# Performance work log

Measured on AMD Instinct MI355X. Metric: run time of the kernel, lower is better.

The kernel has to match this reference:

```python
import jax, jax.numpy as jnp
import numpy as np

BLOCK = 128          # fp8 quantization block size (from linear_deepseek_v3)
FP8_MAX = 448.0      # max representable value of float8_e4m3fn
F8 = jnp.float8_e4m3fn
G, T, K, N = 8, 1024, 7168, 2048


def setup_inputs() -> dict:
    key = jax.random.key(0)
    kx, kw, kb = jax.random.split(key, 3)
    xs = jax.random.normal(kx, (G, T, K), jnp.float32)
    # Build an fp8 block-quantized weight + per-(128x128)-block fp32 scale,
    # matching the stored self.weight (fp8) and self.scale parameters.
    w_raw = jax.random.normal(kw, (G, N, K), jnp.float32)
    wb = w_raw.reshape(G, N // BLOCK, BLOCK, K // BLOCK, BLOCK)
    amax = jnp.max(jnp.abs(wb), axis=(2, 4))            # [G, NB, KB]
    scale = amax / FP8_MAX
    w_q = (wb / scale[:, :, None, :, None]).astype(F8).astype(jnp.float32)
    weight = w_q.reshape(G, N, K)                        # fp8 code values held in fp32
    bias = jax.random.normal(kb, (G, N), jnp.float32) * 0.02
    return {"xs": xs, "weight": weight, "scale": scale, "bias": bias}


def reference(xs, weight, scale, bias):
    """Grouped fp8 block-quantized GEMM with inline dequant.
    xs:     [G, T, K] fp32 activations (one slab per group)
    weight: [G, N, K] fp8-quantized weights (stored as fp32 code values)
    scale:  [G, N/128, K/128] fp32 per-block weight scales
    bias:   [G, N] fp32
    """
    g, t, k = xs.shape
    n = weight.shape[1]
    kb, nb = k // BLOCK, n // BLOCK
    # --- act_quant_deepseek_v3: per (token, 128-col block) absmax/448 scale ---
    xb = xs.reshape(g, t, kb, BLOCK)
    a_scale = jnp.max(jnp.abs(xb), axis=-1) / FP8_MAX        # [G, T, KB]
    x_q = (xb / a_scale[..., None]).astype(F8).astype(jnp.float32)
    x_deq = (x_q * a_scale[..., None]).reshape(g, t, k)      # fused dequant
    # --- weight dequant: broadcast per-(128x128)-block scale ---
    w_deq = (weight.reshape(g, nb, BLOCK, kb, BLOCK)
             * scale[:, :, None, :, None]).reshape(g, n, k)
    # --- grouped GEMM (y = x A^T) + bias, fp32 accumulation ---
    y = jnp.einsum('gtk,gnk->gtn', x_deq, w_deq) + bias[:, None, :]
    return y
```

## Files before the change

kernel.cpp:

```cpp
#include <hip/hip_runtime.h>
#include <hip/hip_bf16.h>
#include <stdint.h>

#define G_ 8
#define T_ 1024
#define K_ 7168
#define N_ 2048
#define KB_ 56
#define NB_ 16
#define NT8_ 56

#define ACT_WGS  57344
#define WREC_WGS 28672

typedef __attribute__((ext_vector_type(4))) float f32x4;
typedef __attribute__((ext_vector_type(8))) int   i32x8;

typedef __attribute__((address_space(3))) uint32_t lds_u32_t;
typedef const __attribute__((address_space(1))) uint32_t gbl_u32_t;

__device__ __forceinline__ void gload_lds16(const void* gsrc, const void* ldst)
{
    __builtin_amdgcn_global_load_lds(
        (gbl_u32_t*)(uintptr_t)gsrc,
        (lds_u32_t*)(uint32_t)(uintptr_t)ldst, 16, 0, 0);
}

__device__ __forceinline__ void blockbar()
{
    asm volatile("" ::: "memory");
    __builtin_amdgcn_s_barrier();
    asm volatile("" ::: "memory");
}

__global__ __launch_bounds__(256) void prep_kernel(
    const float* __restrict__ xs, uint8_t* __restrict__ xq8,
    float* __restrict__ ascale,
    const float* __restrict__ w, uint8_t* __restrict__ wq8)
{
    const int bid = blockIdx.x;
    const int tid = threadIdx.x;
    if (bid < ACT_WGS) {
        const int grp = (bid * 256 + tid) >> 5;
        const int l   = tid & 31;
        const size_t base = (size_t)grp * 128 + (size_t)l * 4;

        const float4 v = *(const float4*)(xs + base);
        float am = fmaxf(fmaxf(fabsf(v.x), fabsf(v.y)),
                         fmaxf(fabsf(v.z), fabsf(v.w)));
#pragma unroll
        for (int off = 1; off <= 16; off <<= 1)
            am = fmaxf(am, __shfl_xor(am, off, 64));

        const float rs = 448.0f / am;
        const float s  = am * (1.0f / 448.0f);

        int pk = __builtin_amdgcn_cvt_pk_fp8_f32(v.x * rs, v.y * rs, 0, false);
        pk     = __builtin_amdgcn_cvt_pk_fp8_f32(v.z * rs, v.w * rs, pk, true);
        *(uint32_t*)(xq8 + base) = (uint32_t)pk;

        if (l == 0) {
            const int kb = grp % KB_;
            const int t  = (grp / KB_) & (T_ - 1);
            const int g  = grp / (KB_ * T_);
            ascale[(((size_t)(g * 4 + (t >> 8))) * KB_ + kb) * 256 + (t & 255)] = s;
        }
    } else {
        const size_t i = ((size_t)(bid - ACT_WGS) * 256 + tid) * 16;
        uint32_t o[4];
#pragma unroll
        for (int q = 0; q < 4; ++q) {
            const float4 a = *(const float4*)(w + i + q * 4);
            int pk = __builtin_amdgcn_cvt_pk_fp8_f32(a.x, a.y, 0, false);
            pk     = __builtin_amdgcn_cvt_pk_fp8_f32(a.z, a.w, pk, true);
            o[q] = (uint32_t)pk;
        }
        *(uint4*)(wq8 + i) = make_uint4(o[0], o[1], o[2], o[3]);
    }
}

union Frag { i32x8 v; struct { int4 lo, hi; } p; };

#define RD_FRAG(dst, base, r)                                                 \
  { const int rx_ = ((r) & 7) << 4;                                           \
    const char* bp_ = smem + (base) + (r)*128;                                \
    dst.p.lo = *(const int4*)(bp_ + ((lhi*32) ^ rx_));                        \
    dst.p.hi = *(const int4*)(bp_ + ((lhi*32 + 16) ^ rx_)); }

#define STG_A(c, t, bb) gload_lds16(pA8[c] + (size_t)(t)*128,                 \
      smem + (bb)*16384 + (c)*4096 + tid*16)
#define STG_B(c, t, bb) gload_lds16(pB8[c] + (size_t)(t)*128,                 \
      smem + 32768 + (bb)*16384 + (c)*4096 + tid*16)
#define STG_S(c) gload_lds16(pS + (size_t)(c)*2048,                           \
      smem + 65536 + ((c)&1)*4096 + tid*16)

__global__ __launch_bounds__(256, 2) void gemm_fp8_kernel(
    const uint8_t* __restrict__ xq8, const uint8_t* __restrict__ wq8,
    const float* __restrict__ ascale, const float* __restrict__ wscale,
    const float* __restrict__ bias, float* __restrict__ y)
{
    __shared__ char smem[73952];

    const int bx0 = blockIdx.x;
    const int g     = bx0 & 7;
    const int inner = bx0 >> 3;
    const int tn    = inner & 15;
    const int tm    = inner >> 4;
    const int t0 = tm * 128, n0 = tn * 128;

    const int tid = threadIdx.x, lane = tid & 63, wid = tid >> 6;
    const int l15 = lane & 15, lhi = lane >> 4;
    const int wrow = (wid >> 1) * 64;
    const int wcol = (wid & 1) * 64;

    const uint8_t* Ag = xq8 + (size_t)g * T_ * K_;
    const uint8_t* Bg = wq8 + (size_t)g * N_ * K_;

    const int srow = tid >> 3;
    const int xoff = ((tid & 7) ^ (srow & 7)) * 16;
    const uint8_t* pA8[4];
    const uint8_t* pB8[4];
#pragma unroll
    for (int c = 0; c < 4; ++c) {
        pA8[c] = Ag + (size_t)(t0 + c * 32 + srow) * K_ + xoff;
        pB8[c] = Bg + (size_t)(n0 + c * 32 + srow) * K_ + xoff;
    }

    const float* pS = ascale + ((size_t)(g * 4 + (tm >> 1)) * KB_) * 256
                    + (tid >> 5) * 256 + (tm & 1) * 128 + (tid & 31) * 4;

    const f32x4 z4 = {0.f, 0.f, 0.f, 0.f};
    f32x4 acc[4][4] = {};
    Frag aF[4], bF[4];
    f32x4 asv[4];

    if (tid < KB_) {
        const float wv = wscale[((size_t)(g * NB_ + tn)) * KB_ + tid];
        *(float*)(smem + 73728 + tid * 4) = wv;
    }
    STG_S(0);
#pragma unroll
    for (int c = 0; c < 4; ++c) { STG_A(c, 0, 0); STG_B(c, 0, 0); }
    asm volatile("s_waitcnt vmcnt(0)" ::: "memory");
    asm volatile("s_waitcnt lgkmcnt(0)" ::: "memory");
    blockbar();

    for (int u = 0; u < NT8_; ++u) {
        const int cur = u & 1, nxt = cur ^ 1;
        const bool pf = (u + 1 < NT8_);
        const int sbuf = (u >> 3) & 1;

        if ((u & 7) == 0 && u + 8 < NT8_) STG_S((u >> 3) + 1);
        if (pf) {
#pragma unroll
            for (int c = 0; c < 4; ++c) { STG_A(c, u + 1, nxt); STG_B(c, u + 1, nxt); }
        }

        const float wsc = *(const float*)(smem + 73728 + u * 4);

#pragma unroll
        for (int n = 0; n < 4; ++n)
            RD_FRAG(bF[n], 32768 + cur * 16384, wcol + n * 16 + l15);
#pragma unroll
        for (int m = 0; m < 4; ++m)
            RD_FRAG(aF[m], cur * 16384, wrow + m * 16 + l15);
#pragma unroll
        for (int m = 0; m < 4; ++m) {
            const float4 sv = *(const float4*)(smem + 65536 + sbuf * 4096 +
                (u & 7) * 512 + (wrow + m * 16 + lhi * 4) * 4);
            asv[m][0] = sv.x * wsc; asv[m][1] = sv.y * wsc;
            asv[m][2] = sv.z * wsc; asv[m][3] = sv.w * wsc;
        }

        __builtin_amdgcn_s_setprio(1);
#pragma unroll
        for (int m = 0; m < 4; ++m) {
#pragma unroll
            for (int n = 0; n < 4; ++n) {
                f32x4 blk = __builtin_amdgcn_mfma_scale_f32_16x16x128_f8f6f4(
                    aF[m].v, bF[n].v, z4, 0, 0, 0, 0x7F7F7F7F, 0, 0x7F7F7F7F);
                acc[m][n] += blk * asv[m];
            }
        }
        __builtin_amdgcn_s_setprio(0);

        if (pf) {
            asm volatile("s_waitcnt vmcnt(0)" ::: "memory");
            blockbar();
        }
    }

    float* Yg = y + (size_t)g * T_ * N_;
#pragma unroll
    for (int n = 0; n < 4; ++n) {
        const int col = n0 + wcol + n * 16 + l15;
        const float bv = bias[g * N_ + col];
#pragma unroll
        for (int m = 0; m < 4; ++m) {
            const int r0 = t0 + wrow + m * 16 + lhi * 4;
#pragma unroll
            for (int j = 0; j < 4; ++j)
                Yg[(size_t)(r0 + j) * N_ + col] = acc[m][n][j] + bv;
        }
    }
}

extern "C" void kernel_launch(void* const* d_in, const int* in_sizes, int n_in,
                              void* d_out, int out_size, void* d_ws, size_t ws_size,
                              hipStream_t stream)
{
    const float* xs     = (const float*)d_in[0];
    const float* weight = (const float*)d_in[1];
    const float* scale  = (const float*)d_in[2];
    const float* bias   = (const float*)d_in[3];
    float* y = (float*)d_out;

    uint8_t* xq8  = (uint8_t*)d_ws;
    float*   ascl = (float*)((char*)d_ws + 58720256);
    uint8_t* wq8  = (uint8_t*)((char*)d_ws + 60555264);

    prep_kernel<<<ACT_WGS + WREC_WGS, 256, 0, stream>>>(
        xs, xq8, ascl, weight, wq8);

    gemm_fp8_kernel<<<G_ * (T_ / 128) * (N_ / 128), 256, 0, stream>>>(
        xq8, wq8, ascl, scale, bias, y);
}
```

Before: 349.2 us.

## Warp-specialize GEMM into producer/consumer waves with triple-buffered LDS

The GEMM block grows to 512 threads. Four producer waves issue the global-to-LDS loads and four consumer waves do the MFMA work, and the LDS ring goes from double to triple buffering with loads issued two steps ahead. The tile order also changes so adjacent blocks share N tiles. The aim is to hide global load latency behind compute. In exchange occupancy drops to one block per CU, LDS use grows, and half the waves never do MFMA work.

After: 326.3 us. -6.5%, faster.

```diff
diff --git a/kernel.cpp b/kernel.cpp
--- a/kernel.cpp
+++ b/kernel.cpp
@@ -88,27 +88,29 @@
     dst.p.hi = *(const int4*)(bp_ + ((lhi*32 + 16) ^ rx_)); }
 
 #define STG_A(c, t, bb) gload_lds16(pA8[c] + (size_t)(t)*128,                 \
-      smem + (bb)*16384 + (c)*4096 + tid*16)
+      smem + (bb)*16384 + (c)*4096 + ptid*16)
 #define STG_B(c, t, bb) gload_lds16(pB8[c] + (size_t)(t)*128,                 \
-      smem + 32768 + (bb)*16384 + (c)*4096 + tid*16)
+      smem + 49152 + (bb)*16384 + (c)*4096 + ptid*16)
 #define STG_S(c) gload_lds16(pS + (size_t)(c)*2048,                           \
-      smem + 65536 + ((c)&1)*4096 + tid*16)
-
-__global__ __launch_bounds__(256, 2) void gemm_fp8_kernel(
+      smem + 98304 + ((c)&1)*4096 + ptid*16)
+
+__global__ __launch_bounds__(512, 1) void gemm_fp8_kernel(
     const uint8_t* __restrict__ xq8, const uint8_t* __restrict__ wq8,
     const float* __restrict__ ascale, const float* __restrict__ wscale,
     const float* __restrict__ bias, float* __restrict__ y)
 {
-    __shared__ char smem[73952];
+    __shared__ char smem[106752];
 
     const int bx0 = blockIdx.x;
     const int g     = bx0 & 7;
     const int inner = bx0 >> 3;
-    const int tn    = inner & 15;
-    const int tm    = inner >> 4;
+    const int tm    = inner & 7;
+    const int tn    = inner >> 3;
     const int t0 = tm * 128, n0 = tn * 128;
 
-    const int tid = threadIdx.x, lane = tid & 63, wid = tid >> 6;
+    const int tid  = threadIdx.x, lane = tid & 63, wid = tid >> 6;
+    const bool producer = (wid >= 4);
+    const int ptid = tid & 255;
     const int l15 = lane & 15, lhi = lane >> 4;
     const int wrow = (wid >> 1) * 64;
     const int wcol = (wid & 1) * 64;
@@ -116,8 +118,8 @@
     const uint8_t* Ag = xq8 + (size_t)g * T_ * K_;
     const uint8_t* Bg = wq8 + (size_t)g * N_ * K_;
 
-    const int srow = tid >> 3;
-    const int xoff = ((tid & 7) ^ (srow & 7)) * 16;
+    const int srow = ptid >> 3;
+    const int xoff = ((ptid & 7) ^ (srow & 7)) * 16;
     const uint8_t* pA8[4];
     const uint8_t* pB8[4];
 #pragma unroll
@@ -125,82 +127,90 @@
         pA8[c] = Ag + (size_t)(t0 + c * 32 + srow) * K_ + xoff;
         pB8[c] = Bg + (size_t)(n0 + c * 32 + srow) * K_ + xoff;
     }
-
     const float* pS = ascale + ((size_t)(g * 4 + (tm >> 1)) * KB_) * 256
-                    + (tid >> 5) * 256 + (tm & 1) * 128 + (tid & 31) * 4;
+                    + (ptid >> 5) * 256 + (tm & 1) * 128 + (ptid & 31) * 4;
 
     const f32x4 z4 = {0.f, 0.f, 0.f, 0.f};
     f32x4 acc[4][4] = {};
-    Frag aF[4], bF[4];
+    Frag bF[4];
     f32x4 asv[4];
 
-    if (tid < KB_) {
-        const float wv = wscale[((size_t)(g * NB_ + tn)) * KB_ + tid];
-        *(float*)(smem + 73728 + tid * 4) = wv;
-    }
-    STG_S(0);
-#pragma unroll
-    for (int c = 0; c < 4; ++c) { STG_A(c, 0, 0); STG_B(c, 0, 0); }
-    asm volatile("s_waitcnt vmcnt(0)" ::: "memory");
-    asm volatile("s_waitcnt lgkmcnt(0)" ::: "memory");
+    if (producer) {
+        if (ptid < KB_) {
+            const float wv = wscale[((size_t)(g * NB_ + tn)) * KB_ + ptid];
+            *(float*)(smem + 106496 + ptid * 4) = wv;
+        }
+        STG_S(0);
+#pragma unroll
+        for (int c = 0; c < 4; ++c) { STG_A(c, 0, 0); STG_B(c, 0, 0); }
+#pragma unroll
+        for (int c = 0; c < 4; ++c) { STG_A(c, 1, 1); STG_B(c, 1, 1); }
+        asm volatile("s_waitcnt vmcnt(8)" ::: "memory");
+    } else {
+        __builtin_amdgcn_s_setprio(1);
+    }
     blockbar();
 
+    int cur = 0;
     for (int u = 0; u < NT8_; ++u) {
-        const int cur = u & 1, nxt = cur ^ 1;
-        const bool pf = (u + 1 < NT8_);
         const int sbuf = (u >> 3) & 1;
 
-        if ((u & 7) == 0 && u + 8 < NT8_) STG_S((u >> 3) + 1);
-        if (pf) {
-#pragma unroll
-            for (int c = 0; c < 4; ++c) { STG_A(c, u + 1, nxt); STG_B(c, u + 1, nxt); }
-        }
-
-        const float wsc = *(const float*)(smem + 73728 + u * 4);
-
-#pragma unroll
-        for (int n = 0; n < 4; ++n)
-            RD_FRAG(bF[n], 32768 + cur * 16384, wcol + n * 16 + l15);
-#pragma unroll
-        for (int m = 0; m < 4; ++m)
-            RD_FRAG(aF[m], cur * 16384, wrow + m * 16 + l15);
-#pragma unroll
-        for (int m = 0; m < 4; ++m) {
-            const float4 sv = *(const float4*)(smem + 65536 + sbuf * 4096 +
-                (u & 7) * 512 + (wrow + m * 16 + lhi * 4) * 4);
-            asv[m][0] = sv.x * wsc; asv[m][1] = sv.y * wsc;
-            asv[m][2] = sv.z * wsc; asv[m][3] = sv.w * wsc;
-        }
-
-        __builtin_amdgcn_s_setprio(1);
-#pragma unroll
-        for (int m = 0; m < 4; ++m) {
-#pragma unroll
-            for (int n = 0; n < 4; ++n) {
-                f32x4 blk = __builtin_amdgcn_mfma_scale_f32_16x16x128_f8f6f4(
-                    aF[m].v, bF[n].v, z4, 0, 0, 0, 0x7F7F7F7F, 0, 0x7F7F7F7F);
-                acc[m][n] += blk * asv[m];
-            }
-        }
-        __builtin_amdgcn_s_setprio(0);
-
-        if (pf) {
-            asm volatile("s_waitcnt vmcnt(0)" ::: "memory");
-            blockbar();
-        }
-    }
-
-    float* Yg = y + (size_t)g * T_ * N_;
-#pragma unroll
-    for (int n = 0; n < 4; ++n) {
-        const int col = n0 + wcol + n * 16 + l15;
-        const float bv = bias[g * N_ + col];
-#pragma unroll
-        for (int m = 0; m < 4; ++m) {
-            const int r0 = t0 + wrow + m * 16 + lhi * 4;
-#pragma unroll
-            for (int j = 0; j < 4; ++j)
-                Yg[(size_t)(r0 + j) * N_ + col] = acc[m][n][j] + bv;
+        if (producer) {
+            if ((u & 7) == 0 && u + 8 < NT8_) STG_S((u >> 3) + 1);
+            if (u + 2 < NT8_) {
+                const int fb = (cur + 2 >= 3) ? cur - 1 : cur + 2;
+#pragma unroll
+                for (int c = 0; c < 4; ++c) { STG_A(c, u + 2, fb); STG_B(c, u + 2, fb); }
+                asm volatile("s_waitcnt vmcnt(8)" ::: "memory");
+            } else {
+                asm volatile("s_waitcnt vmcnt(0)" ::: "memory");
+            }
+        } else {
+            const float wsc = *(const float*)(smem + 106496 + u * 4);
+            const int abase = cur * 16384;
+            const int bbase = 49152 + cur * 16384;
+
+#pragma unroll
+            for (int n = 0; n < 4; ++n)
+                RD_FRAG(bF[n], bbase, wcol + n * 16 + l15);
+#pragma unroll
+            for (int m = 0; m < 4; ++m) {
+                const float4 sv = *(const float4*)(smem + 98304 + sbuf * 4096 +
+                    (u & 7) * 512 + (wrow + m * 16 + lhi * 4) * 4);
+                asv[m][0] = sv.x * wsc; asv[m][1] = sv.y * wsc;
+                asv[m][2] = sv.z * wsc; asv[m][3] = sv.w * wsc;
+            }
+
+#pragma unroll
+            for (int m = 0; m < 4; ++m) {
+                Frag aF;
+                RD_FRAG(aF, abase, wrow + m * 16 + l15);
+#pragma unroll
+                for (int n = 0; n < 4; ++n) {
+                    f32x4 blk = __builtin_amdgcn_mfma_scale_f32_16x16x128_f8f6f4(
+                        aF.v, bF[n].v, z4, 0, 0, 0, 0x7F7F7F7F, 0, 0x7F7F7F7F);
+                    acc[m][n] += blk * asv[m];
+                }
+            }
+        }
+
+        blockbar();
+        cur = (cur + 1 >= 3) ? 0 : cur + 1;
+    }
+
+    if (!producer) {
+        float* Yg = y + (size_t)g * T_ * N_;
+#pragma unroll
+        for (int n = 0; n < 4; ++n) {
+            const int col = n0 + wcol + n * 16 + l15;
+            const float bv = bias[g * N_ + col];
+#pragma unroll
+            for (int m = 0; m < 4; ++m) {
+                const int r0 = t0 + wrow + m * 16 + lhi * 4;
+#pragma unroll
+                for (int j = 0; j < 4; ++j)
+                    Yg[(size_t)(r0 + j) * N_ + col] = acc[m][n][j] + bv;
+            }
         }
     }
 }
@@ -222,6 +232,6 @@
     prep_kernel<<<ACT_WGS + WREC_WGS, 256, 0, stream>>>(
         xs, xq8, ascl, weight, wq8);
 
-    gemm_fp8_kernel<<<G_ * (T_ / 128) * (N_ / 128), 256, 0, stream>>>(
+    gemm_fp8_kernel<<<G_ * (T_ / 128) * (N_ / 128), 512, 0, stream>>>(
         xq8, wq8, ascl, scale, bias, y);
 }
```
